# Kernel tuning notes

Hardware: AMD Instinct MI355X
Metric: run time of the kernel (lower is better)

Reference implementation:

```python
import jax, jax.numpy as jnp
import numpy as np
from jax import lax

STATE_DIM = 16
HIDDEN_DIM = 128
ALIVE_THRESH = 0.1


def _maxpool3(a):
    # 3x3 max pool, stride 1, padding 1 (pad value -inf, matching torch max_pool2d)
    return lax.reduce_window(a, -jnp.inf, lax.max,
                             (1, 1, 3, 3), (1, 1, 1, 1),
                             ((0, 0), (0, 0), (1, 1), (1, 1)))


def _make_dw_kernel(state_dim):
    # fixed perception kernel: identity, sobel-x, sobel-y per channel
    identity = np.outer([0, 1, 0], [0, 1, 0])
    dx = np.outer([1, 2, 1], [-1, 0, 1]) / 8.0
    kernel = np.stack([identity, dx, dx.T], axis=0)          # (3,3,3)
    kernel = np.tile(kernel, [state_dim, 1, 1])              # (3*state_dim,3,3)
    return jnp.asarray(kernel[:, None, :, :], dtype=jnp.float32)  # OIHW (48,1,3,3)


def setup_inputs() -> dict:
    key = jax.random.key(0)
    kx, k2, k3 = jax.random.split(key, 3)
    x = jax.random.normal(kx, (8, STATE_DIM, 96, 96), dtype=jnp.float32)
    # learned 1x1 conv weights (torch inits w3 to zero; random here for a
    w2 = jax.random.normal(k2, (HIDDEN_DIM, 3 * STATE_DIM), dtype=jnp.float32) * 0.05
    w3 = jax.random.normal(k3, (STATE_DIM, HIDDEN_DIM), dtype=jnp.float32) * 0.05
    return {"x": x, "num_steps": 24, "dw_kernel": _make_dw_kernel(STATE_DIM),
            "w2": w2, "w3": w3}


def reference(x, num_steps, dw_kernel, w2, w3):
    def update(x):
        # depthwise 3x3 perception conv: groups = STATE_DIM, 16 -> 48 channels
        y = lax.conv_general_dilated(
            x, dw_kernel, window_strides=(1, 1), padding=((1, 1), (1, 1)),
            dimension_numbers=('NCHW', 'OIHW', 'NCHW'),
            feature_group_count=STATE_DIM)
        h = jax.nn.relu(jnp.einsum('oc,bchw->bohw', w2, y))   # 1x1 conv + relu
        return jnp.einsum('oc,bchw->bohw', w3, h)             # 1x1 conv

    def alive(alpha):
        return _maxpool3(alpha) > ALIVE_THRESH

    keys = jax.random.split(jax.random.key(42), num_steps)

    def step(x, k):
        alive_pre = alive(x[:, 3:4])                          # (B,1,H,W) bool
        upd_mask = jax.random.uniform(k, x.shape) > 0.5
        x = x + upd_mask.astype(x.dtype) * update(x)
        x = x * (alive_pre & alive(x[:, 3:4])).astype(x.dtype)
        return x, x

    _, frames = lax.scan(step, x, keys)                       # (T,B,C,H,W)
    return frames
```

## Files before the change

kernel.cpp:

```cpp
#include <hip/hip_runtime.h>
#include <cstdint>
#include <cstddef>

#define T_STEPS 24
#define BATCH 8
#define CHN 16
#define HH 96
#define WW 96
#define HW (HH*WW)
#define NPIX (BATCH*HW)
#define NELEM (BATCH*CHN*HW)
#define NBLK 1152

typedef float f32x2 __attribute__((ext_vector_type(2)));

__host__ __device__ inline void tf2x32(uint32_t k0, uint32_t k1,
                                       uint32_t x0, uint32_t x1,
                                       uint32_t& o0, uint32_t& o1) {
  const uint32_t ks2 = k0 ^ k1 ^ 0x1BD11BDAu;
  uint32_t v0 = x0 + k0, v1 = x1 + k1;
#define RR(d) { v0 += v1; v1 = (v1 << (d)) | (v1 >> (32 - (d))); v1 ^= v0; }
  RR(13) RR(15) RR(26) RR(6)
  v0 += k1;  v1 += ks2 + 1u;
  RR(17) RR(29) RR(16) RR(24)
  v0 += ks2; v1 += k0 + 2u;
  RR(13) RR(15) RR(26) RR(6)
  v0 += k0;  v1 += k1 + 3u;
  RR(17) RR(29) RR(16) RR(24)
  v0 += k1;  v1 += ks2 + 4u;
  RR(13) RR(15) RR(26) RR(6)
  v0 += ks2; v1 += k0 + 5u;
#undef RR
  o0 = v0; o1 = v1;
}

__global__ __launch_bounds__(256) void wt_transpose(
    const float* __restrict__ w2, const float* __restrict__ w3,
    float* __restrict__ w2t, float* __restrict__ w3t)
{
  const int idx = blockIdx.x * 256 + threadIdx.x;
  if (idx < 6144) {
    const int k = idx >> 7, h = idx & 127;
    w2t[idx] = w2[h * 48 + k];
  } else {
    const int i = idx - 6144;
    const int o = i >> 4, cc = i & 15;
    w3t[i] = w3[cc * 128 + o];
  }
}

template <bool MASK>
__global__ __launch_bounds__(256, 4) void nca_step(
    const float* __restrict__ xin,
    float* __restrict__ frames_prev,
    const uint8_t* __restrict__ alive_prev,
    float* __restrict__ xnew,
    uint8_t* __restrict__ alive_cur,
    const float* __restrict__ w2t, const float* __restrict__ w3t,
    uint32_t k0, uint32_t k1)
{
  __shared__ float smem[4096];
  float* y_t = smem;
  float (*part)[4][64] = (float (*)[4][64])smem;

  const int tid  = threadIdx.x;
  const int lane = tid & 63;
  const int sub  = __builtin_amdgcn_readfirstlane(tid >> 6);
  const int bid  = blockIdx.x;
  const int vbid = (bid & 7) * 144 + (bid >> 3);
  const int P    = vbid * 64;
  const int b    = P / HW;
  const int p0   = P - b * HW;
  const int p    = p0 + lane;
  const int r    = p / WW;
  const int c    = p - r * WW;
  const bool rn = r > 0, rs = r < HH - 1, cw = c > 0, ce = c < WW - 1;

  float f[9];
  #pragma unroll
  for (int i = 0; i < 9; ++i) f[i] = 1.f;
  if constexpr (MASK) {
    const float* x3 = xin + ((size_t)(b * CHN + 3)) * HW + p;
    const uint8_t* ap = alive_prev + (size_t)b * HW + p;
    const bool rvs[5] = { r > 1, rn, true, rs, r < HH - 2 };
    const bool cvs[5] = { c > 1, cw, true, ce, c < WW - 2 };
    float hm[5][3];
    #pragma unroll
    for (int i = 0; i < 5; ++i) {
      const int off = (i - 2) * WW;
      const bool rv = rvs[i];
      const float a0 = (rv && cvs[0]) ? x3[off - 2] : 0.f;
      const float a1 = (rv && cvs[1]) ? x3[off - 1] : 0.f;
      const float a2 =  rv            ? x3[off]     : 0.f;
      const float a3 = (rv && cvs[3]) ? x3[off + 1] : 0.f;
      const float a4 = (rv && cvs[4]) ? x3[off + 2] : 0.f;
      hm[i][0] = fmaxf(fmaxf(a0, a1), a2);
      hm[i][1] = fmaxf(fmaxf(a1, a2), a3);
      hm[i][2] = fmaxf(fmaxf(a2, a3), a4);
    }
    #pragma unroll
    for (int qr = 0; qr < 3; ++qr)
      #pragma unroll
      for (int qc = 0; qc < 3; ++qc) {
        const float mp = fmaxf(fmaxf(hm[qr][qc], hm[qr + 1][qc]),
                               hm[qr + 2][qc]);
        const bool inb = rvs[qr + 1] && cvs[qc + 1];
        const uint8_t al = inb ? ap[(qr - 1) * WW + (qc - 1)] : (uint8_t)0;
        f[qr * 3 + qc] = (inb && al && (mp > 0.1f)) ? 1.f : 0.f;
      }
  }

  float n11m[4];
  #pragma unroll
  for (int cq = 0; cq < 4; ++cq) {
    const int ch = sub * 4 + cq;
    const size_t jb = ((size_t)(b * CHN + ch)) * HW + p;
    const float* xc = xin + jb;
    float n00 = (rn && cw) ? xc[-WW - 1] : 0.f;
    float n01 = rn         ? xc[-WW]     : 0.f;
    float n02 = (rn && ce) ? xc[-WW + 1] : 0.f;
    float n10 = cw         ? xc[-1]      : 0.f;
    float n11 =              xc[0];
    float n12 = ce         ? xc[1]       : 0.f;
    float n20 = (rs && cw) ? xc[WW - 1]  : 0.f;
    float n21 = rs         ? xc[WW]      : 0.f;
    float n22 = (rs && ce) ? xc[WW + 1]  : 0.f;
    if constexpr (MASK) {
      n00 *= f[0]; n01 *= f[1]; n02 *= f[2];
      n10 *= f[3]; n11 *= f[4]; n12 *= f[5];
      n20 *= f[6]; n21 *= f[7]; n22 *= f[8];
      frames_prev[jb] = n11;
    }
    n11m[cq] = n11;
    y_t[(3 * ch + 0) * 66 + lane] = n11;
    y_t[(3 * ch + 1) * 66 + lane] =
        ((n02 + n22 - n00 - n20) + 2.f * (n12 - n10)) * 0.125f;
    y_t[(3 * ch + 2) * 66 + lane] =
        ((n20 + n22 - n00 - n02) + 2.f * (n21 - n01)) * 0.125f;
    if (ch == 3) {
      float m = fmaxf(fmaxf(fmaxf(n00, n01), fmaxf(n02, n10)),
                      fmaxf(fmaxf(n11, n12), fmaxf(n20, n21)));
      m = fmaxf(m, n22);
      alive_cur[P + lane] = (m > 0.1f) ? 1 : 0;
    }
  }

  float keep[4];
  #pragma unroll
  for (int i = 0; i < 4; ++i) {
    const int cc = sub * 4 + i;
    const uint32_t j = (uint32_t)((b * CHN + cc) * HW + p);
    uint32_t o0, o1;
    tf2x32(k0, k1, 0u, j, o0, o1);
    const uint32_t bits = o0 ^ o1;
    keep[i] = ((bits >> 9) > 0x400000u) ? 1.f : 0.f;
  }

  __syncthreads();

  float yv[48];
  #pragma unroll
  for (int k = 0; k < 48; ++k)
    yv[k] = y_t[k * 66 + lane];

  f32x2 acc[16];
  #pragma unroll
  for (int j = 0; j < 16; ++j) acc[j] = (f32x2){0.f, 0.f};

  const f32x2* w2b2 = (const f32x2*)(w2t + sub * 32);
  #pragma unroll
  for (int k = 0; k < 48; ++k) {
    const f32x2 yv2 = {yv[k], yv[k]};
    const f32x2* w2r = w2b2 + k * 64;
    #pragma unroll
    for (int j = 0; j < 16; ++j)
      acc[j] = __builtin_elementwise_fma(w2r[j], yv2, acc[j]);
  }

  f32x2 o2[8];
  #pragma unroll
  for (int i = 0; i < 8; ++i) o2[i] = (f32x2){0.f, 0.f};

  const f32x2* w3b2 = (const f32x2*)(w3t + (size_t)sub * 32 * 16);
  #pragma unroll
  for (int hh = 0; hh < 32; ++hh) {
    const float av = (hh & 1) ? acc[hh >> 1].y : acc[hh >> 1].x;
    const float hv = fmaxf(av, 0.f);
    const f32x2 hv2 = {hv, hv};
    const f32x2* w3r = w3b2 + hh * 8;
    #pragma unroll
    for (int n = 0; n < 8; ++n)
      o2[n] = __builtin_elementwise_fma(w3r[n], hv2, o2[n]);
  }

  __syncthreads();

  #pragma unroll
  for (int cc = 0; cc < CHN; ++cc)
    part[cc][sub][lane] = (cc & 1) ? o2[cc >> 1].y : o2[cc >> 1].x;
  __syncthreads();

  #pragma unroll
  for (int i = 0; i < 4; ++i) {
    const int cc = sub * 4 + i;
    const float s = (part[cc][0][lane] + part[cc][1][lane]) +
                    (part[cc][2][lane] + part[cc][3][lane]);
    const uint32_t j = (uint32_t)((b * CHN + cc) * HW + p);
    xnew[j] = n11m[i] + keep[i] * s;
  }
}

__global__ __launch_bounds__(256) void nca_mask(
    const float* __restrict__ xnew, const uint8_t* __restrict__ alive_pre,
    float* __restrict__ xout)
{
  const int lane = threadIdx.x & 63;
  const int quad = threadIdx.x >> 6;
  const int bid  = blockIdx.x;
  const int vbid = (bid & 7) * 144 + (bid >> 3);
  const int pix  = vbid * 64 + lane;
  const int b = pix / HW;
  const int p = pix - b * HW;
  const int r = p / WW;
  const int c = p - r * WW;
  const bool rn = r > 0, rs = r < HH - 1, cw = c > 0, ce = c < WW - 1;

  const float* x3 = xnew + ((size_t)b * CHN + 3) * HW + p;
  float m = x3[0];
  if (rn) {
    m = fmaxf(m, x3[-WW]);
    if (cw) m = fmaxf(m, x3[-WW - 1]);
    if (ce) m = fmaxf(m, x3[-WW + 1]);
  }
  if (cw) m = fmaxf(m, x3[-1]);
  if (ce) m = fmaxf(m, x3[1]);
  if (rs) {
    m = fmaxf(m, x3[WW]);
    if (cw) m = fmaxf(m, x3[WW - 1]);
    if (ce) m = fmaxf(m, x3[WW + 1]);
  }
  const float f = ((m > 0.1f) && alive_pre[pix]) ? 1.f : 0.f;

  const size_t base = ((size_t)b * CHN + quad * 4) * HW + p;
  #pragma unroll
  for (int i = 0; i < 4; ++i)
    xout[base + (size_t)i * HW] = xnew[base + (size_t)i * HW] * f;
}

extern "C" void kernel_launch(void* const* d_in, const int* in_sizes, int n_in,
                              void* d_out, int out_size, void* d_ws, size_t ws_size,
                              hipStream_t stream) {
  const float* x0 = (const float*)d_in[0];
  const float* w2 = (const float*)d_in[3];
  const float* w3 = (const float*)d_in[4];
  float* out = (float*)d_out;

  char* ws = (char*)d_ws;
  float*   xlast  = (float*)ws;
  uint8_t* aliveA = (uint8_t*)(ws + (size_t)NELEM * 4);
  uint8_t* aliveB = aliveA + NPIX;
  float*   w3t    = (float*)(ws + (size_t)NELEM * 4 + 2 * (size_t)NPIX);
  float*   w2t    = w3t + 2048;

  uint32_t keys[T_STEPS][2];
  for (int t = 0; t < T_STEPS; ++t) {
    uint32_t a, b;
    tf2x32(0u, 42u, 0u, (uint32_t)t, a, b);
    keys[t][0] = a; keys[t][1] = b;
  }

  wt_transpose<<<32, 256, 0, stream>>>(w2, w3, w2t, w3t);

  nca_step<false><<<NBLK, 256, 0, stream>>>(
      x0, nullptr, nullptr, out + (size_t)1 * NELEM, aliveA, w2t, w3t,
      keys[0][0], keys[0][1]);

  for (int t = 1; t < T_STEPS; ++t) {
    const float* xin  = out + (size_t)t * NELEM;
    float* frames_prv = out + (size_t)(t - 1) * NELEM;
    float* xdst = (t < T_STEPS - 1) ? out + (size_t)(t + 1) * NELEM : xlast;
    const uint8_t* aprev = (t & 1) ? aliveA : aliveB;
    uint8_t*       acur  = (t & 1) ? aliveB : aliveA;
    nca_step<true><<<NBLK, 256, 0, stream>>>(
        xin, frames_prv, aprev, xdst, acur, w2t, w3t,
        keys[t][0], keys[t][1]);
  }

  nca_mask<<<NBLK, 256, 0, stream>>>(
      xlast, (T_STEPS & 1) ? aliveA : aliveB,
      out + (size_t)(T_STEPS - 1) * NELEM);
}
```

Before: 662.5 us.

## Compute first 1x1 conv with split-bf16 MFMA instead of fp32 FMAs

Moves the 48->128 hidden-layer matmul onto MFMA bf16 instructions. Both activations and weights are split into three bf16 terms, and six cross-product MFMAs recover near-fp32 accuracy. Weights are prepacked into fragment layout once. Perception outputs are written to LDS as bf16 planes, and the hidden result goes through LDS for the fp32 second layer. It adds LDS traffic, an extra barrier and larger shared memory, which may reduce occupancy, in exchange for fewer VALU FMAs.

```diff
diff --git a/kernel.cpp b/kernel.cpp
--- a/kernel.cpp
+++ b/kernel.cpp
@@ -13,6 +13,22 @@
 #define NBLK 1152
 
 typedef float f32x2 __attribute__((ext_vector_type(2)));
+typedef float f32x4 __attribute__((ext_vector_type(4)));
+typedef short bf16x8 __attribute__((ext_vector_type(8)));
+
+#define YS_ROW 144
+#define YS_PLANE 9216
+#define H_STRIDE 68
+#define SMEM_BYTES 34816
+
+__device__ __host__ inline uint16_t bf16r(float x) {
+  union { float f; uint32_t u; } v; v.f = x;
+  v.u += 0x7FFFu + ((v.u >> 16) & 1u);
+  return (uint16_t)(v.u >> 16);
+}
+__device__ __host__ inline float bf16f(uint16_t h) {
+  union { float f; uint32_t u; } v; v.u = ((uint32_t)h) << 16; return v.f;
+}
 
 __host__ __device__ inline void tf2x32(uint32_t k0, uint32_t k1,
                                        uint32_t x0, uint32_t x1,
@@ -34,16 +50,28 @@
   o0 = v0; o1 = v1;
 }
 
-__global__ __launch_bounds__(256) void wt_transpose(
+__global__ __launch_bounds__(256) void wt_prep(
     const float* __restrict__ w2, const float* __restrict__ w3,
-    float* __restrict__ w2t, float* __restrict__ w3t)
+    float* __restrict__ w3t, uint16_t* __restrict__ wfrag)
 {
   const int idx = blockIdx.x * 256 + threadIdx.x;
-  if (idx < 6144) {
-    const int k = idx >> 7, h = idx & 127;
-    w2t[idx] = w2[h * 48 + k];
+  if (idx < 24576) {
+    const int j  = idx & 7;
+    const int l  = (idx >> 3) & 63;
+    const int kt = (idx >> 9) & 1;
+    const int tn = (idx >> 10) & 7;
+    const int s  = idx >> 13;
+    const int h  = tn * 16 + (l & 15);
+    const int k  = kt * 32 + ((l >> 4) & 3) * 8 + j;
+    float v = (k < 48) ? w2[h * 48 + k] : 0.f;
+    const uint16_t t0 = bf16r(v);
+    const float r1 = v - bf16f(t0);
+    const uint16_t t1 = bf16r(r1);
+    const float r2 = r1 - bf16f(t1);
+    const uint16_t t2 = bf16r(r2);
+    wfrag[idx] = (s == 0) ? t0 : (s == 1) ? t1 : t2;
   } else {
-    const int i = idx - 6144;
+    const int i = idx - 24576;
     const int o = i >> 4, cc = i & 15;
     w3t[i] = w3[cc * 128 + o];
   }
@@ -56,12 +84,12 @@
     const uint8_t* __restrict__ alive_prev,
     float* __restrict__ xnew,
     uint8_t* __restrict__ alive_cur,
-    const float* __restrict__ w2t, const float* __restrict__ w3t,
+    const uint16_t* __restrict__ wfrag, const float* __restrict__ w3t,
     uint32_t k0, uint32_t k1)
 {
-  __shared__ float smem[4096];
-  float* y_t = smem;
-  float (*part)[4][64] = (float (*)[4][64])smem;
+  __shared__ char smemRaw[SMEM_BYTES];
+  float* h_ld = (float*)smemRaw;
+  float (*part)[4][64] = (float (*)[4][64])smemRaw;
 
   const int tid  = threadIdx.x;
   const int lane = tid & 63;
@@ -111,6 +139,7 @@
   }
 
   float n11m[4];
+  float yv[12];
   #pragma unroll
   for (int cq = 0; cq < 4; ++cq) {
     const int ch = sub * 4 + cq;
@@ -132,17 +161,42 @@
       frames_prev[jb] = n11;
     }
     n11m[cq] = n11;
-    y_t[(3 * ch + 0) * 66 + lane] = n11;
-    y_t[(3 * ch + 1) * 66 + lane] =
-        ((n02 + n22 - n00 - n20) + 2.f * (n12 - n10)) * 0.125f;
-    y_t[(3 * ch + 2) * 66 + lane] =
-        ((n20 + n22 - n00 - n02) + 2.f * (n21 - n01)) * 0.125f;
+    yv[cq * 3 + 0] = n11;
+    yv[cq * 3 + 1] = ((n02 + n22 - n00 - n20) + 2.f * (n12 - n10)) * 0.125f;
+    yv[cq * 3 + 2] = ((n20 + n22 - n00 - n02) + 2.f * (n21 - n01)) * 0.125f;
     if (ch == 3) {
       float m = fmaxf(fmaxf(fmaxf(n00, n01), fmaxf(n02, n10)),
                       fmaxf(fmaxf(n11, n12), fmaxf(n20, n21)));
       m = fmaxf(m, n22);
       alive_cur[P + lane] = (m > 0.1f) ? 1 : 0;
     }
+  }
+
+  {
+    uint16_t u0[12], u1[12], u2[12];
+    #pragma unroll
+    for (int i = 0; i < 12; ++i) {
+      const float v = yv[i];
+      u0[i] = bf16r(v);
+      const float r1v = v - bf16f(u0[i]);
+      u1[i] = bf16r(r1v);
+      u2[i] = bf16r(r1v - bf16f(u1[i]));
+    }
+    const int rowoff = lane * YS_ROW + sub * 24;
+    #pragma unroll
+    for (int q = 0; q < 3; ++q) {
+      *(ushort4*)(smemRaw + 0 * YS_PLANE + rowoff + q * 8) =
+          make_ushort4(u0[q*4+0], u0[q*4+1], u0[q*4+2], u0[q*4+3]);
+      *(ushort4*)(smemRaw + 1 * YS_PLANE + rowoff + q * 8) =
+          make_ushort4(u1[q*4+0], u1[q*4+1], u1[q*4+2], u1[q*4+3]);
+      *(ushort4*)(smemRaw + 2 * YS_PLANE + rowoff + q * 8) =
+          make_ushort4(u2[q*4+0], u2[q*4+1], u2[q*4+2], u2[q*4+3]);
+    }
+    const int zoff = lane * YS_ROW + 96 + sub * 8;
+    const ushort4 z = make_ushort4(0, 0, 0, 0);
+    *(ushort4*)(smemRaw + 0 * YS_PLANE + zoff) = z;
+    *(ushort4*)(smemRaw + 1 * YS_PLANE + zoff) = z;
+    *(ushort4*)(smemRaw + 2 * YS_PLANE + zoff) = z;
   }
 
   float keep[4];
@@ -158,24 +212,60 @@
 
   __syncthreads();
 
-  float yv[48];
-  #pragma unroll
-  for (int k = 0; k < 48; ++k)
-    yv[k] = y_t[k * 66 + lane];
-
-  f32x2 acc[16];
-  #pragma unroll
-  for (int j = 0; j < 16; ++j) acc[j] = (f32x2){0.f, 0.f};
-
-  const f32x2* w2b2 = (const f32x2*)(w2t + sub * 32);
-  #pragma unroll
-  for (int k = 0; k < 48; ++k) {
-    const f32x2 yv2 = {yv[k], yv[k]};
-    const f32x2* w2r = w2b2 + k * 64;
-    #pragma unroll
-    for (int j = 0; j < 16; ++j)
-      acc[j] = __builtin_elementwise_fma(w2r[j], yv2, acc[j]);
-  }
+  const int lm = lane & 15;
+  const int hq = lane >> 4;
+  f32x4 acc[4][2];
+  #pragma unroll
+  for (int m = 0; m < 4; ++m)
+    #pragma unroll
+    for (int t2 = 0; t2 < 2; ++t2) acc[m][t2] = (f32x4){0.f, 0.f, 0.f, 0.f};
+
+  #pragma unroll
+  for (int kt = 0; kt < 2; ++kt) {
+    bf16x8 bfr[2][3];
+    #pragma unroll
+    for (int t2 = 0; t2 < 2; ++t2)
+      #pragma unroll
+      for (int s = 0; s < 3; ++s) {
+        const int tn = sub * 2 + t2;
+        bfr[t2][s] = *(const bf16x8*)(wfrag +
+            (size_t)(((s * 8 + tn) * 2 + kt) * 64 + lane) * 8);
+      }
+    #pragma unroll
+    for (int m = 0; m < 4; ++m) {
+      bf16x8 af[3];
+      #pragma unroll
+      for (int s = 0; s < 3; ++s)
+        af[s] = *(const bf16x8*)(smemRaw + s * YS_PLANE +
+                                 (m * 16 + lm) * YS_ROW + kt * 64 + hq * 16);
+      #pragma unroll
+      for (int t2 = 0; t2 < 2; ++t2) {
+        acc[m][t2] = __builtin_amdgcn_mfma_f32_16x16x32_bf16(
+            af[2], bfr[t2][0], acc[m][t2], 0, 0, 0);
+        acc[m][t2] = __builtin_amdgcn_mfma_f32_16x16x32_bf16(
+            af[1], bfr[t2][1], acc[m][t2], 0, 0, 0);
+        acc[m][t2] = __builtin_amdgcn_mfma_f32_16x16x32_bf16(
+            af[0], bfr[t2][2], acc[m][t2], 0, 0, 0);
+        acc[m][t2] = __builtin_amdgcn_mfma_f32_16x16x32_bf16(
+            af[1], bfr[t2][0], acc[m][t2], 0, 0, 0);
+        acc[m][t2] = __builtin_amdgcn_mfma_f32_16x16x32_bf16(
+            af[0], bfr[t2][1], acc[m][t2], 0, 0, 0);
+        acc[m][t2] = __builtin_amdgcn_mfma_f32_16x16x32_bf16(
+            af[0], bfr[t2][0], acc[m][t2], 0, 0, 0);
+      }
+    }
+  }
+
+  __syncthreads();
+
+  #pragma unroll
+  for (int m = 0; m < 4; ++m)
+    #pragma unroll
+    for (int t2 = 0; t2 < 2; ++t2) {
+      const int hd = (sub * 2 + t2) * 16 + lm;
+      const int px = m * 16 + hq * 4;
+      *(f32x4*)(h_ld + hd * H_STRIDE + px) = acc[m][t2];
+    }
 
   f32x2 o2[8];
   #pragma unroll
@@ -184,8 +274,7 @@
   const f32x2* w3b2 = (const f32x2*)(w3t + (size_t)sub * 32 * 16);
   #pragma unroll
   for (int hh = 0; hh < 32; ++hh) {
-    const float av = (hh & 1) ? acc[hh >> 1].y : acc[hh >> 1].x;
-    const float hv = fmaxf(av, 0.f);
+    const float hv = fmaxf(h_ld[(sub * 32 + hh) * H_STRIDE + lane], 0.f);
     const f32x2 hv2 = {hv, hv};
     const f32x2* w3r = w3b2 + hh * 8;
     #pragma unroll
@@ -256,11 +345,11 @@
   float* out = (float*)d_out;
 
   char* ws = (char*)d_ws;
-  float*   xlast  = (float*)ws;
-  uint8_t* aliveA = (uint8_t*)(ws + (size_t)NELEM * 4);
-  uint8_t* aliveB = aliveA + NPIX;
-  float*   w3t    = (float*)(ws + (size_t)NELEM * 4 + 2 * (size_t)NPIX);
-  float*   w2t    = w3t + 2048;
+  float*    xlast  = (float*)ws;
+  uint8_t*  aliveA = (uint8_t*)(ws + (size_t)NELEM * 4);
+  uint8_t*  aliveB = aliveA + NPIX;
+  float*    w3t    = (float*)(ws + (size_t)NELEM * 4 + 2 * (size_t)NPIX);
+  uint16_t* wfrag  = (uint16_t*)((char*)w3t + 8192);
 
   uint32_t keys[T_STEPS][2];
   for (int t = 0; t < T_STEPS; ++t) {
@@ -269,10 +358,10 @@
     keys[t][0] = a; keys[t][1] = b;
   }
 
-  wt_transpose<<<32, 256, 0, stream>>>(w2, w3, w2t, w3t);
+  wt_prep<<<104, 256, 0, stream>>>(w2, w3, w3t, wfrag);
 
   nca_step<false><<<NBLK, 256, 0, stream>>>(
-      x0, nullptr, nullptr, out + (size_t)1 * NELEM, aliveA, w2t, w3t,
+      x0, nullptr, nullptr, out + (size_t)1 * NELEM, aliveA, wfrag, w3t,
       keys[0][0], keys[0][1]);
 
   for (int t = 1; t < T_STEPS; ++t) {
@@ -282,7 +371,7 @@
     const uint8_t* aprev = (t & 1) ? aliveA : aliveB;
     uint8_t*       acur  = (t & 1) ? aliveB : aliveA;
     nca_step<true><<<NBLK, 256, 0, stream>>>(
-        xin, frames_prv, aprev, xdst, acur, w2t, w3t,
+        xin, frames_prv, aprev, xdst, acur, wfrag, w3t,
         keys[t][0], keys[t][1]);
   }
 
```

Result: faster. 611.1 us (-7.8%).
